# Performance work log

Hardware: AMD Instinct MI355X
Metric: run time of the kernel (lower is better)

## Reference

```python
import jax, jax.numpy as jnp
import numpy as np

B, S, E, H = 2, 2048, 1024, 16
DK = E // H


def setup_inputs() -> dict:
    key = jax.random.key(0)
    ks = jax.random.split(key, 10)
    x = jax.random.normal(ks[0], (B, S, E), dtype=jnp.float32)
    mask = jax.random.randint(ks[1], (B, S, S), 0, 2).astype(bool)
    scale = 1.0 / np.sqrt(E)
    def lin(k):
        kw, kb = jax.random.split(k)
        W = jax.random.uniform(kw, (E, E), minval=-scale, maxval=scale, dtype=jnp.float32)
        b = jax.random.uniform(kb, (E,), minval=-scale, maxval=scale, dtype=jnp.float32)
        return W, b
    Wq, bq = lin(ks[2])
    Wk, bk = lin(ks[3])
    Wv, bv = lin(ks[4])
    Wo, bo = lin(ks[5])
    return {"x": x, "mask": mask, "Wq": Wq, "bq": bq, "Wk": Wk, "bk": bk,
            "Wv": Wv, "bv": bv, "Wo": Wo, "bo": bo}


def reference(x, mask, Wq, bq, Wk, bk, Wv, bv, Wo, bo):
    # projections (torch Linear: y = x @ W.T + b)
    q = x @ Wq.T + bq
    k = x @ Wk.T + bk
    v = x @ Wv.T + bv
    # separate heads: [B,S,E] -> [B,H,S,DK]
    def split(t):
        return t.reshape(B, S, H, DK).transpose(0, 2, 1, 3)
    q, k, v = split(q), split(k), split(v)
    scores = jnp.einsum("bhqd,bhkd->bhqk", q, k) / jnp.sqrt(jnp.float32(DK))
    # masked_fill: positions where mask is True get -1e9 (mask broadcast over heads)
    scores = jnp.where(mask[:, None, :, :], jnp.float32(-1e9), scores)
    attn = jax.nn.softmax(scores, axis=-1)  # dropout is identity in eval
    out = jnp.einsum("bhqk,bhkd->bhqd", attn, v)
    out = out.transpose(0, 2, 1, 3).reshape(B, S, E)  # combine heads
    return out @ Wo.T + bo
```

## Files before the change

kernel.cpp:

```cpp
#include <hip/hip_runtime.h>
#include <hip/hip_bf16.h>


typedef __attribute__((ext_vector_type(8))) short short8;
typedef __attribute__((ext_vector_type(4))) short s16x4;
typedef __attribute__((ext_vector_type(4))) float f32x4;

#define MFMA16(a, b, c) __builtin_amdgcn_mfma_f32_16x16x32_bf16(a, b, c, 0, 0, 0)

#define BATCH 2
#define SEQ   2048
#define EMB   1024
#define HEADS 16
#define DKK   64
#define MROWS (BATCH * SEQ)

typedef __hip_bfloat16 bf16;
typedef unsigned long long u64;

static __device__ __forceinline__ short bf16b(float f) {
    union { bf16 h; short s; } u;
    u.h = __float2bfloat16(f);
    return u.s;
}
static __device__ __forceinline__ short8 ld8k(const bf16* p) {
    return *(const short8*)p;
}
static __device__ __forceinline__ short8 ld8kf(const float* p) {
    const f32x4 a = *(const f32x4*)p;
    const f32x4 b = *(const f32x4*)(p + 4);
    short8 r;
    r[0] = bf16b(a[0]); r[1] = bf16b(a[1]); r[2] = bf16b(a[2]); r[3] = bf16b(a[3]);
    r[4] = bf16b(b[0]); r[5] = bf16b(b[1]); r[6] = bf16b(b[2]); r[7] = bf16b(b[3]);
    return r;
}

static __device__ __forceinline__ void glds16(const bf16* g, bf16* l) {
    __builtin_amdgcn_global_load_lds(
        (const __attribute__((address_space(1))) void*)g,
        (__attribute__((address_space(3))) void*)l, 16, 0, 0);
}

__global__ void detect_kernel(const unsigned int* __restrict__ mw,
                              int* __restrict__ flags) {
    __shared__ int mbyte;
    if (threadIdx.x == 0) mbyte = 0;
    __syncthreads();
    int mb = 0;
    for (int i = threadIdx.x; i < 4096; i += 256)
        if (mw[i] > 1u) mb = 1;
    if (mb) atomicOr(&mbyte, 1);
    __syncthreads();
    if (threadIdx.x == 0) { flags[0] = 1; flags[1] = mbyte; }
}

__global__ __launch_bounds__(256) void pack_mask(
        const void* __restrict__ mp, u64* __restrict__ bm,
        const int* __restrict__ flags) {
    const bool m8 = flags[1] != 0;
    const unsigned char* p8 = (const unsigned char*)mp;
    const int* p32 = (const int*)mp;
    const int lane = threadIdx.x & 63;
    const int w = (blockIdx.x * 256 + threadIdx.x) >> 6;
#pragma unroll 4
    for (int i = 0; i < 32; ++i) {
        const int L = i * 4096 + w;
        const size_t e = (size_t)L * 64 + lane;
        const bool v = m8 ? (p8[e] != 0) : (p32[e] != 0);
        const u64 bal = __ballot(v);
        if (lane == 0) {
            const int qg = L >> 5, it = L & 31;
            bm[((qg >> 11) * 32 + it) * 2048 + (qg & 2047)] = bal;
        }
    }
}

__global__ __launch_bounds__(256) void cvt_all(
        const float* __restrict__ x,  const float* __restrict__ wq,
        const float* __restrict__ wk, const float* __restrict__ wv,
        const float* __restrict__ wo,
        bf16* __restrict__ xb,  bf16* __restrict__ wqb,
        bf16* __restrict__ wkb, bf16* __restrict__ wvb,
        bf16* __restrict__ wob) {
    const int bid = blockIdx.x;
    const float* s; bf16* d; int base;
    if (bid < 2048)      { s = x;  d = xb;  base = bid; }
    else if (bid < 2560) { s = wq; d = wqb; base = bid - 2048; }
    else if (bid < 3072) { s = wk; d = wkb; base = bid - 2560; }
    else if (bid < 3584) { s = wv; d = wvb; base = bid - 3072; }
    else                 { s = wo; d = wob; base = bid - 3584; }
    const int i = (base * 256 + threadIdx.x) * 8;
    *(short8*)(d + i) = ld8kf(s + i);
}

__global__ __launch_bounds__(256) void gemm_qkv_staged(
        const bf16* __restrict__ X,
        const bf16* __restrict__ Wq, const bf16* __restrict__ Wk,
        const bf16* __restrict__ Wv,
        const float* __restrict__ bq, const float* __restrict__ bk,
        const float* __restrict__ bv,
        bf16* __restrict__ qo, bf16* __restrict__ ko, bf16* __restrict__ vo) {
    __shared__ bf16 As[2][128 * 32];
    __shared__ bf16 Bs[2][128 * 32];

    const int t = threadIdx.x, lane = t & 63;
    const int wv = t >> 6;
    const int mb = blockIdx.x / 24, nb = blockIdx.x % 24;
    const int m0 = mb * 128;
    const int n0g = nb * 128;
    const int sel = n0g >> 10;
    const int n0 = n0g & 1023;
    const bf16* W     = sel == 0 ? Wq : (sel == 1 ? Wk : Wv);
    const float* bias = sel == 0 ? bq : (sel == 1 ? bk : bv);
    bf16* out         = sel == 0 ? qo : (sel == 1 ? ko : vo);
    const float oscale = sel == 0 ? 0.18033688011f : 1.0f;

    const int wr = wv >> 1, wc = wv & 1;
    const int m_off = wr * 64, n_off = wc * 64;
    const int l16 = lane & 15, quad = lane >> 4;

    int srow[2], sg[2];
#pragma unroll
    for (int i = 0; i < 2; ++i) {
        const int c = i * 256 + t;
        srow[i] = c >> 2;
        sg[i]   = (c & 3) ^ (srow[i] & 3);
    }

    f32x4 acc[4][4];
#pragma unroll
    for (int i = 0; i < 4; ++i)
#pragma unroll
        for (int j = 0; j < 4; ++j)
            acc[i][j] = (f32x4){0.f, 0.f, 0.f, 0.f};

#pragma unroll
    for (int i = 0; i < 2; ++i) {
        glds16(X + (m0 + srow[i]) * 1024 + sg[i] * 8, &As[0][(i * 256 + t) * 8]);
        glds16(W + (n0 + srow[i]) * 1024 + sg[i] * 8, &Bs[0][(i * 256 + t) * 8]);
    }

    for (int it = 0; it < 32; ++it) {
        __syncthreads();
        if (it < 31) {
            const int ktn = (it + 1) * 32;
            const int nb_ = (it + 1) & 1;
#pragma unroll
            for (int i = 0; i < 2; ++i) {
                glds16(X + (m0 + srow[i]) * 1024 + ktn + sg[i] * 8,
                       &As[nb_][(i * 256 + t) * 8]);
                glds16(W + (n0 + srow[i]) * 1024 + ktn + sg[i] * 8,
                       &Bs[nb_][(i * 256 + t) * 8]);
            }
        }
        const bf16* Ab = As[it & 1];
        const bf16* Bb = Bs[it & 1];
        short8 af[4], bfr[4];
#pragma unroll
        for (int ii = 0; ii < 4; ++ii) {
            const int row = m_off + ii * 16 + l16;
            const int slot = quad ^ (row & 3);
            af[ii] = *(const short8*)(Ab + row * 32 + slot * 8);
        }
#pragma unroll
        for (int jj = 0; jj < 4; ++jj) {
            const int row = n_off + jj * 16 + l16;
            const int slot = quad ^ (row & 3);
            bfr[jj] = *(const short8*)(Bb + row * 32 + slot * 8);
        }
#pragma unroll
        for (int ii = 0; ii < 4; ++ii)
#pragma unroll
            for (int jj = 0; jj < 4; ++jj)
                acc[ii][jj] = MFMA16(af[ii], bfr[jj], acc[ii][jj]);
    }

#pragma unroll
    for (int j = 0; j < 4; ++j) {
        const int nl = n0 + n_off + j * 16 + l16;
        const float bj = bias[nl];
        const int h = nl >> 6, d = nl & 63;
#pragma unroll
        for (int i = 0; i < 4; ++i) {
#pragma unroll
            for (int r = 0; r < 4; ++r) {
                const int m = m0 + m_off + i * 16 + quad * 4 + r;
                const float v = (acc[i][j][r] + bj) * oscale;
                const int bb = m >> 11, ss = m & 2047;
                const int idx = (sel == 2)
                    ? ((bb * HEADS + h) * DKK + d) * SEQ + ss
                    : ((bb * HEADS + h) * SEQ + ss) * DKK + d;
                out[idx] = __float2bfloat16(v);
            }
        }
    }
}

__global__ __launch_bounds__(256) void gemm_out_staged(
        const bf16* __restrict__ X,
        const bf16* __restrict__ W, const float* __restrict__ bias,
        float* __restrict__ out) {
    __shared__ bf16 As[2][128 * 32];
    __shared__ bf16 Bs[2][64 * 32];

    const int t = threadIdx.x, lane = t & 63;
    const int wv = t >> 6;
    const int mb = blockIdx.x >> 4, nb = blockIdx.x & 15;
    const int m0 = mb * 128, n0 = nb * 64;
    const int wr = wv >> 1, wc = wv & 1;
    const int m_off = wr * 64, n_off = wc * 32;
    const int l16 = lane & 15, quad = lane >> 4;

    int srow[2], sg[2];
#pragma unroll
    for (int i = 0; i < 2; ++i) {
        const int c = i * 256 + t;
        srow[i] = c >> 2;
        sg[i]   = (c & 3) ^ (srow[i] & 3);
    }
    const int brow = t >> 2;
    const int bslot = (t & 3) ^ (brow & 3);

    f32x4 acc[4][2];
#pragma unroll
    for (int i = 0; i < 4; ++i)
#pragma unroll
        for (int j = 0; j < 2; ++j)
            acc[i][j] = (f32x4){0.f, 0.f, 0.f, 0.f};

#pragma unroll
    for (int i = 0; i < 2; ++i)
        glds16(X + (m0 + srow[i]) * 1024 + sg[i] * 8, &As[0][(i * 256 + t) * 8]);
    glds16(W + (n0 + brow) * 1024 + bslot * 8, &Bs[0][t * 8]);

    for (int it = 0; it < 32; ++it) {
        __syncthreads();
        if (it < 31) {
            const int ktn = (it + 1) * 32;
            const int nb_ = (it + 1) & 1;
#pragma unroll
            for (int i = 0; i < 2; ++i)
                glds16(X + (m0 + srow[i]) * 1024 + ktn + sg[i] * 8,
                       &As[nb_][(i * 256 + t) * 8]);
            glds16(W + (n0 + brow) * 1024 + ktn + bslot * 8, &Bs[nb_][t * 8]);
        }
        const bf16* Ab = As[it & 1];
        const bf16* Bb = Bs[it & 1];
        short8 af[4], bfr[2];
#pragma unroll
        for (int ii = 0; ii < 4; ++ii) {
            const int row = m_off + ii * 16 + l16;
            const int slot = quad ^ (row & 3);
            af[ii] = *(const short8*)(Ab + row * 32 + slot * 8);
        }
#pragma unroll
        for (int jj = 0; jj < 2; ++jj) {
            const int row = n_off + jj * 16 + l16;
            const int slot = quad ^ (row & 3);
            bfr[jj] = *(const short8*)(Bb + row * 32 + slot * 8);
        }
#pragma unroll
        for (int ii = 0; ii < 4; ++ii)
#pragma unroll
            for (int jj = 0; jj < 2; ++jj)
                acc[ii][jj] = MFMA16(af[ii], bfr[jj], acc[ii][jj]);
    }

#pragma unroll
    for (int j = 0; j < 2; ++j) {
        const int n = n0 + n_off + j * 16 + l16;
        const float bj = bias[n];
#pragma unroll
        for (int i = 0; i < 4; ++i) {
#pragma unroll
            for (int r = 0; r < 4; ++r) {
                const int m = m0 + m_off + i * 16 + quad * 4 + r;
                out[m * 1024 + n] = acc[i][j][r] + bj;
            }
        }
    }
}

__global__ __launch_bounds__(256, 2) void attn_kernel(
        const bf16* __restrict__ Qw,
        const bf16* __restrict__ Kw,
        const bf16* __restrict__ Vw,
        const u64* __restrict__ bmT,
        bf16* __restrict__ attn_out) {
    const int t = threadIdx.x;
    const int lane = t & 63;
    const int wv   = t >> 6;
    const int l16 = lane & 15, quad = lane >> 4;
    const int h = blockIdx.y, b = blockIdx.z;
    const int bh = b * HEADS + h;
    const int qb0 = blockIdx.x * 128;

    const bf16* Q  = Qw + bh * SEQ * DKK;
    const bf16* Kp = Kw + bh * SEQ * DKK;
    const bf16* Vt = Vw + bh * DKK * SEQ;

    __shared__ bf16 Ks[2][4096];
    __shared__ bf16 Vs[2][4096];
    __shared__ bf16 lds_p[4][2][16][72];

    short8 qf[2][2];
#pragma unroll
    for (int i = 0; i < 2; ++i)
#pragma unroll
        for (int t2 = 0; t2 < 2; ++t2)
            qf[i][t2] = ld8k(Q + (qb0 + wv * 32 + i * 16 + l16) * DKK + t2 * 32 + quad * 8);

    f32x4 o[2][4];
#pragma unroll
    for (int i = 0; i < 2; ++i)
#pragma unroll
        for (int jd = 0; jd < 4; ++jd) o[i][jd] = (f32x4){0.f, 0.f, 0.f, 0.f};
    float lsum[2] = {0.f, 0.f};

    int srow[2], sg[2];
#pragma unroll
    for (int i = 0; i < 2; ++i) {
        const int c = i * 256 + t;
        srow[i] = c >> 3;
        sg[i]   = (c & 7) ^ (srow[i] & 7);
    }

#pragma unroll
    for (int i = 0; i < 2; ++i)
        glds16(Kp + srow[i] * DKK + sg[i] * 8, &Ks[0][(i * 256 + t) * 8]);
#pragma unroll
    for (int i = 0; i < 2; ++i)
        glds16(Vt + srow[i] * SEQ + sg[i] * 8, &Vs[0][(i * 256 + t) * 8]);

    const int qlane0 = qb0 + wv * 32 + l16;
    u64 mc[2];
#pragma unroll
    for (int i = 0; i < 2; ++i)
        mc[i] = bmT[(size_t)(b * 32) * 2048 + qlane0 + i * 16];

    for (int it = 0; it < SEQ / 64; ++it) {
        __syncthreads();
        const int nb_ = (it + 1) & 1;
        if (it < SEQ / 64 - 1) {
            const int ktn = (it + 1) * 64;
#pragma unroll
            for (int i = 0; i < 2; ++i)
                glds16(Kp + (ktn + srow[i]) * DKK + sg[i] * 8, &Ks[nb_][(i * 256 + t) * 8]);
#pragma unroll
            for (int i = 0; i < 2; ++i)
                glds16(Vt + srow[i] * SEQ + ktn + sg[i] * 8, &Vs[nb_][(i * 256 + t) * 8]);
        }
        u64 mn[2];
        if (it < SEQ / 64 - 1) {
#pragma unroll
            for (int i = 0; i < 2; ++i)
                mn[i] = bmT[(size_t)(b * 32 + it + 1) * 2048 + qlane0 + i * 16];
        }

        const bf16* Kb = Ks[it & 1];
        const bf16* Vb = Vs[it & 1];

        short8 kf[2][4];
#pragma unroll
        for (int t2 = 0; t2 < 2; ++t2)
#pragma unroll
            for (int j = 0; j < 4; ++j) {
                const int row = j * 16 + l16;
                const int slot = (t2 * 4 + quad) ^ (row & 7);
                kf[t2][j] = *(const short8*)(Kb + row * 64 + slot * 8);
            }

        f32x4 s[2][4];
#pragma unroll
        for (int i = 0; i < 2; ++i)
#pragma unroll
            for (int j = 0; j < 4; ++j) {
                s[i][j] = (f32x4){0.f, 0.f, 0.f, 0.f};
#pragma unroll
                for (int t2 = 0; t2 < 2; ++t2)
                    s[i][j] = MFMA16(kf[t2][j], qf[i][t2], s[i][j]);
            }

#pragma unroll
        for (int i = 0; i < 2; ++i) {
            const unsigned wlo = (unsigned)mc[i];
            const unsigned whi = (unsigned)(mc[i] >> 32);
#pragma unroll
            for (int j = 0; j < 4; ++j) {
                const unsigned half = (j < 2) ? wlo : whi;
                const int bp0 = (j & 1) * 16 + quad * 4;
                float p[4];
#pragma unroll
                for (int r = 0; r < 4; ++r) {
                    const float bit = (float)((half >> (bp0 + r)) & 1u);
                    const float p_ = __builtin_exp2f(__builtin_fmaf(bit, -1000.f, s[i][j][r]));
                    p[r] = p_;
                    lsum[i] += p_;
                }
                s16x4 pk;
                pk[0] = bf16b(p[0]); pk[1] = bf16b(p[1]);
                pk[2] = bf16b(p[2]); pk[3] = bf16b(p[3]);
                *(s16x4*)(&lds_p[wv][i][l16][j * 16 + quad * 4]) = pk;
            }
        }

#pragma unroll
        for (int t2 = 0; t2 < 2; ++t2) {
            short8 vf[4];
#pragma unroll
            for (int jd = 0; jd < 4; ++jd) {
                const int row = jd * 16 + l16;
                const int slot = (t2 * 4 + quad) ^ (row & 7);
                vf[jd] = *(const short8*)(Vb + row * 64 + slot * 8);
            }
#pragma unroll
            for (int i = 0; i < 2; ++i) {
                short8 pf = *(const short8*)(&lds_p[wv][i][l16][t2 * 32 + quad * 8]);
#pragma unroll
                for (int jd = 0; jd < 4; ++jd)
                    o[i][jd] = MFMA16(pf, vf[jd], o[i][jd]);
            }
        }
        if (it < SEQ / 64 - 1) {
#pragma unroll
            for (int i = 0; i < 2; ++i) mc[i] = mn[i];
        }
    }

#pragma unroll
    for (int i = 0; i < 2; ++i) {
        float l = lsum[i];
        l += __shfl_xor(l, 16, 64);
        l += __shfl_xor(l, 32, 64);
        lsum[i] = l;
    }
#pragma unroll
    for (int i = 0; i < 2; ++i)
#pragma unroll
        for (int r = 0; r < 4; ++r) {
            const float inv = 1.0f / __shfl(lsum[i], quad * 4 + r, 64);
            const int q = qb0 + wv * 32 + i * 16 + quad * 4 + r;
#pragma unroll
            for (int jd = 0; jd < 4; ++jd)
                attn_out[(b * SEQ + q) * EMB + h * DKK + jd * 16 + l16] =
                    __float2bfloat16(o[i][jd][r] * inv);
        }
}

extern "C" void kernel_launch(void* const* d_in, const int* in_sizes, int n_in,
                              void* d_out, int out_size, void* d_ws, size_t ws_size,
                              hipStream_t stream) {
    char* ws = (char*)d_ws;
    const size_t MB = 1024 * 1024;
    int*  flags = (int*)ws;
    u64*  bm    = (u64*)(ws + 256);
    bf16* xb    = (bf16*)(ws + 256 + MB);
    bf16* wqb   = (bf16*)(ws + 256 + 9 * MB);
    bf16* wkb   = (bf16*)(ws + 256 + 11 * MB);
    bf16* wvb   = (bf16*)(ws + 256 + 13 * MB);
    bf16* wob   = (bf16*)(ws + 256 + 15 * MB);
    bf16* k_ws  = (bf16*)(ws + 256 + 17 * MB);
    bf16* attn_ws = xb;

    bf16* q_ws = (bf16*)d_out;
    bf16* v_ws = (bf16*)d_out + 4194304;

    detect_kernel<<<1, 256, 0, stream>>>((const unsigned int*)d_in[1], flags);
    pack_mask<<<1024, 256, 0, stream>>>(d_in[1], bm, flags);

    cvt_all<<<4096, 256, 0, stream>>>(
        (const float*)d_in[0], (const float*)d_in[2], (const float*)d_in[4],
        (const float*)d_in[6], (const float*)d_in[8],
        xb, wqb, wkb, wvb, wob);

    gemm_qkv_staged<<<768, 256, 0, stream>>>(
        xb, wqb, wkb, wvb,
        (const float*)d_in[3], (const float*)d_in[5], (const float*)d_in[7],
        q_ws, k_ws, v_ws);

    attn_kernel<<<dim3(SEQ / 128, HEADS, BATCH), 256, 0, stream>>>(
        q_ws, k_ws, v_ws, bm, attn_ws);

    gemm_out_staged<<<512, 256, 0, stream>>>(
        attn_ws, wob, (const float*)d_in[9], (float*)d_out);
}
```

Before: 262.9 us.

## Split attention work across 8 waves with 16 query rows each, MFMA row sums

The attention kernel now runs 512 threads per block, so each of 8 waves owns 16 query rows instead of 32. K/V tile staging is spread over more threads, with one load each. The softmax denominator is now accumulated with an extra MFMA against a vector of ones instead of scalar adds and cross-lane shuffles. This cuts per-wave register pressure and raises occupancy, at the cost of reading the K and V fragments from LDS twice as often per query row and one extra MFMA per step.

```diff
diff --git a/kernel.cpp b/kernel.cpp
--- a/kernel.cpp
+++ b/kernel.cpp
@@ -281,7 +281,7 @@
     }
 }
 
-__global__ __launch_bounds__(256, 2) void attn_kernel(
+__global__ __launch_bounds__(512, 4) void attn_kernel(
         const bf16* __restrict__ Qw,
         const bf16* __restrict__ Kw,
         const bf16* __restrict__ Vw,
@@ -301,61 +301,44 @@
 
     __shared__ bf16 Ks[2][4096];
     __shared__ bf16 Vs[2][4096];
-    __shared__ bf16 lds_p[4][2][16][72];
-
-    short8 qf[2][2];
-#pragma unroll
-    for (int i = 0; i < 2; ++i)
-#pragma unroll
-        for (int t2 = 0; t2 < 2; ++t2)
-            qf[i][t2] = ld8k(Q + (qb0 + wv * 32 + i * 16 + l16) * DKK + t2 * 32 + quad * 8);
-
-    f32x4 o[2][4];
-#pragma unroll
-    for (int i = 0; i < 2; ++i)
-#pragma unroll
-        for (int jd = 0; jd < 4; ++jd) o[i][jd] = (f32x4){0.f, 0.f, 0.f, 0.f};
-    float lsum[2] = {0.f, 0.f};
-
-    int srow[2], sg[2];
-#pragma unroll
-    for (int i = 0; i < 2; ++i) {
-        const int c = i * 256 + t;
-        srow[i] = c >> 3;
-        sg[i]   = (c & 7) ^ (srow[i] & 7);
-    }
-
-#pragma unroll
-    for (int i = 0; i < 2; ++i)
-        glds16(Kp + srow[i] * DKK + sg[i] * 8, &Ks[0][(i * 256 + t) * 8]);
-#pragma unroll
-    for (int i = 0; i < 2; ++i)
-        glds16(Vt + srow[i] * SEQ + sg[i] * 8, &Vs[0][(i * 256 + t) * 8]);
-
-    const int qlane0 = qb0 + wv * 32 + l16;
-    u64 mc[2];
-#pragma unroll
-    for (int i = 0; i < 2; ++i)
-        mc[i] = bmT[(size_t)(b * 32) * 2048 + qlane0 + i * 16];
+    __shared__ bf16 lds_p[8][16][72];
+
+    short8 qf[2];
+#pragma unroll
+    for (int t2 = 0; t2 < 2; ++t2)
+        qf[t2] = ld8k(Q + (qb0 + wv * 16 + l16) * DKK + t2 * 32 + quad * 8);
+
+    const short ob = bf16b(1.0f);
+    short8 ones;
+#pragma unroll
+    for (int e = 0; e < 8; ++e) ones[e] = ob;
+
+    f32x4 o[4];
+#pragma unroll
+    for (int jd = 0; jd < 4; ++jd) o[jd] = (f32x4){0.f, 0.f, 0.f, 0.f};
+    f32x4 lacc = (f32x4){0.f, 0.f, 0.f, 0.f};
+    const f32x4 zacc = (f32x4){0.f, 0.f, 0.f, 0.f};
+
+    const int srow = t >> 3;
+    const int sg   = (t & 7) ^ (srow & 7);
+
+    glds16(Kp + srow * DKK + sg * 8, &Ks[0][t * 8]);
+    glds16(Vt + srow * SEQ + sg * 8, &Vs[0][t * 8]);
+
+    const int qlane = qb0 + wv * 16 + l16;
+    u64 mc = bmT[(size_t)(b * 32) * 2048 + qlane];
 
     for (int it = 0; it < SEQ / 64; ++it) {
         __syncthreads();
         const int nb_ = (it + 1) & 1;
         if (it < SEQ / 64 - 1) {
             const int ktn = (it + 1) * 64;
-#pragma unroll
-            for (int i = 0; i < 2; ++i)
-                glds16(Kp + (ktn + srow[i]) * DKK + sg[i] * 8, &Ks[nb_][(i * 256 + t) * 8]);
-#pragma unroll
-            for (int i = 0; i < 2; ++i)
-                glds16(Vt + srow[i] * SEQ + ktn + sg[i] * 8, &Vs[nb_][(i * 256 + t) * 8]);
-        }
-        u64 mn[2];
-        if (it < SEQ / 64 - 1) {
-#pragma unroll
-            for (int i = 0; i < 2; ++i)
-                mn[i] = bmT[(size_t)(b * 32 + it + 1) * 2048 + qlane0 + i * 16];
-        }
+            glds16(Kp + (ktn + srow) * DKK + sg * 8, &Ks[nb_][t * 8]);
+            glds16(Vt + srow * SEQ + ktn + sg * 8, &Vs[nb_][t * 8]);
+        }
+        u64 mn;
+        if (it < SEQ / 64 - 1)
+            mn = bmT[(size_t)(b * 32 + it + 1) * 2048 + qlane];
 
         const bf16* Kb = Ks[it & 1];
         const bf16* Vb = Vs[it & 1];
@@ -370,38 +353,27 @@
                 kf[t2][j] = *(const short8*)(Kb + row * 64 + slot * 8);
             }
 
-        f32x4 s[2][4];
-#pragma unroll
-        for (int i = 0; i < 2; ++i)
-#pragma unroll
-            for (int j = 0; j < 4; ++j) {
-                s[i][j] = (f32x4){0.f, 0.f, 0.f, 0.f};
-#pragma unroll
-                for (int t2 = 0; t2 < 2; ++t2)
-                    s[i][j] = MFMA16(kf[t2][j], qf[i][t2], s[i][j]);
-            }
-
-#pragma unroll
-        for (int i = 0; i < 2; ++i) {
-            const unsigned wlo = (unsigned)mc[i];
-            const unsigned whi = (unsigned)(mc[i] >> 32);
-#pragma unroll
-            for (int j = 0; j < 4; ++j) {
-                const unsigned half = (j < 2) ? wlo : whi;
-                const int bp0 = (j & 1) * 16 + quad * 4;
-                float p[4];
-#pragma unroll
-                for (int r = 0; r < 4; ++r) {
-                    const float bit = (float)((half >> (bp0 + r)) & 1u);
-                    const float p_ = __builtin_exp2f(__builtin_fmaf(bit, -1000.f, s[i][j][r]));
-                    p[r] = p_;
-                    lsum[i] += p_;
-                }
-                s16x4 pk;
-                pk[0] = bf16b(p[0]); pk[1] = bf16b(p[1]);
-                pk[2] = bf16b(p[2]); pk[3] = bf16b(p[3]);
-                *(s16x4*)(&lds_p[wv][i][l16][j * 16 + quad * 4]) = pk;
-            }
+        f32x4 s[4];
+#pragma unroll
+        for (int j = 0; j < 4; ++j) {
+            s[j] = MFMA16(kf[0][j], qf[0], zacc);
+            s[j] = MFMA16(kf[1][j], qf[1], s[j]);
+        }
+
+        const unsigned wlo = (unsigned)mc;
+        const unsigned whi = (unsigned)(mc >> 32);
+#pragma unroll
+        for (int j = 0; j < 4; ++j) {
+            const unsigned half = (j < 2) ? wlo : whi;
+            const int bp0 = (j & 1) * 16 + quad * 4;
+            s16x4 pk;
+#pragma unroll
+            for (int r = 0; r < 4; ++r) {
+                const float bit = (float)((half >> (bp0 + r)) & 1u);
+                const float p_ = __builtin_exp2f(__builtin_fmaf(bit, -1000.f, s[j][r]));
+                pk[r] = bf16b(p_);
+            }
+            *(s16x4*)(&lds_p[wv][l16][j * 16 + quad * 4]) = pk;
         }
 
 #pragma unroll
@@ -413,38 +385,24 @@
                 const int slot = (t2 * 4 + quad) ^ (row & 7);
                 vf[jd] = *(const short8*)(Vb + row * 64 + slot * 8);
             }
-#pragma unroll
-            for (int i = 0; i < 2; ++i) {
-                short8 pf = *(const short8*)(&lds_p[wv][i][l16][t2 * 32 + quad * 8]);
-#pragma unroll
-                for (int jd = 0; jd < 4; ++jd)
-                    o[i][jd] = MFMA16(pf, vf[jd], o[i][jd]);
-            }
-        }
-        if (it < SEQ / 64 - 1) {
-#pragma unroll
-            for (int i = 0; i < 2; ++i) mc[i] = mn[i];
-        }
-    }
-
-#pragma unroll
-    for (int i = 0; i < 2; ++i) {
-        float l = lsum[i];
-        l += __shfl_xor(l, 16, 64);
-        l += __shfl_xor(l, 32, 64);
-        lsum[i] = l;
-    }
-#pragma unroll
-    for (int i = 0; i < 2; ++i)
-#pragma unroll
-        for (int r = 0; r < 4; ++r) {
-            const float inv = 1.0f / __shfl(lsum[i], quad * 4 + r, 64);
-            const int q = qb0 + wv * 32 + i * 16 + quad * 4 + r;
+            const short8 pf = *(const short8*)(&lds_p[wv][l16][t2 * 32 + quad * 8]);
+            lacc = MFMA16(pf, ones, lacc);
 #pragma unroll
             for (int jd = 0; jd < 4; ++jd)
-                attn_out[(b * SEQ + q) * EMB + h * DKK + jd * 16 + l16] =
-                    __float2bfloat16(o[i][jd][r] * inv);
-        }
+                o[jd] = MFMA16(pf, vf[jd], o[jd]);
+        }
+        if (it < SEQ / 64 - 1) mc = mn;
+    }
+
+#pragma unroll
+    for (int r = 0; r < 4; ++r) {
+        const float inv = 1.0f / lacc[r];
+        const int q = qb0 + wv * 16 + quad * 4 + r;
+#pragma unroll
+        for (int jd = 0; jd < 4; ++jd)
+            attn_out[(b * SEQ + q) * EMB + h * DKK + jd * 16 + l16] =
+                __float2bfloat16(o[jd][r] * inv);
+    }
 }
 
 extern "C" void kernel_launch(void* const* d_in, const int* in_sizes, int n_in,
@@ -478,7 +436,7 @@
         (const float*)d_in[3], (const float*)d_in[5], (const float*)d_in[7],
         q_ws, k_ws, v_ws);
 
-    attn_kernel<<<dim3(SEQ / 128, HEADS, BATCH), 256, 0, stream>>>(
+    attn_kernel<<<dim3(SEQ / 128, HEADS, BATCH), 512, 0, stream>>>(
         q_ws, k_ws, v_ws, bm, attn_ws);
 
     gemm_out_staged<<<512, 256, 0, stream>>>(
```

Result: no change. 264.4 us (+0.6%).
